# Performance work log

Measured on AMD Instinct MI355X. Metric: run time of the kernel, lower is better.

## Reference

```python
import jax, jax.numpy as jnp
import numpy as np

N_NODES = 100000
N_EDGES = 1600000
IN_FEATS = 128
N_HIDDEN = 128
N_CLASSES = 47


def _glorot(key, shape):
    lim = float(np.sqrt(6.0 / (shape[0] + shape[1])))
    return jax.random.uniform(key, shape, jnp.float32, -lim, lim)


def setup_inputs() -> dict:
    key = jax.random.key(0)
    ks = jax.random.split(key, 9)
    x = jax.random.normal(ks[0], (N_NODES, IN_FEATS), jnp.float32)
    src = jax.random.randint(ks[1], (N_EDGES,), 0, N_NODES, jnp.int32)
    dst = jax.random.randint(ks[2], (N_EDGES,), 0, N_NODES, jnp.int32)
    return {
        "x": x,
        "W_self_0": _glorot(ks[3], (IN_FEATS, N_HIDDEN)),
        "W_neigh_0": _glorot(ks[4], (IN_FEATS, N_HIDDEN)),
        "W_self_1": _glorot(ks[5], (N_HIDDEN, N_HIDDEN)),
        "W_neigh_1": _glorot(ks[6], (N_HIDDEN, N_HIDDEN)),
        "W_self_2": _glorot(ks[7], (N_HIDDEN, N_CLASSES)),
        "W_neigh_2": _glorot(ks[8], (N_HIDDEN, N_CLASSES)),
        "src": src,
        "dst": dst,
    }


def _sage_layer(h, src, dst, W_self, W_neigh):
    # mean aggregation of in-neighbor features (DGL SAGEConv 'mean', no bias)
    neigh_sum = jax.ops.segment_sum(h[src], dst, num_segments=N_NODES)  # [N, d]
    deg = jax.ops.segment_sum(jnp.ones((src.shape[0],), h.dtype), dst,
                              num_segments=N_NODES)  # [N]
    h_neigh = neigh_sum / jnp.maximum(deg, 1.0)[:, None]
    return h @ W_self + h_neigh @ W_neigh


def reference(x, W_self_0, W_neigh_0, W_self_1, W_neigh_1, W_self_2, W_neigh_2,
              src, dst):
    h = _sage_layer(x, src, dst, W_self_0, W_neigh_0)
    h = jax.nn.relu(h)  # dropout is identity in eval/reference mode
    h = _sage_layer(h, src, dst, W_self_1, W_neigh_1)
    h = jax.nn.relu(h)
    h = _sage_layer(h, src, dst, W_self_2, W_neigh_2)
    return h
```

## Files before the change

### kernel.cpp

```cpp
#include <hip/hip_runtime.h>
#include <hip/hip_bf16.h>

#define NN 100000
#define NE 1600000
#define NBK 196

typedef __attribute__((ext_vector_type(8))) short bf16x8;
typedef __attribute__((ext_vector_type(4))) float f32x4;

__device__ __forceinline__ unsigned short f2bf(float x) {
    unsigned u = __float_as_uint(x);
    return (unsigned short)((u + 0x7fffu + ((u >> 16) & 1u)) >> 16);
}
__device__ __forceinline__ float bflo(unsigned v) { return __uint_as_float(v << 16); }
__device__ __forceinline__ float bfhi(unsigned v) { return __uint_as_float(v & 0xffff0000u); }

#define ACCV(A, v) do { \
    A[0] += bflo((v).x); A[1] += bfhi((v).x); \
    A[2] += bflo((v).y); A[3] += bfhi((v).y); \
    A[4] += bflo((v).z); A[5] += bfhi((v).z); \
    A[6] += bflo((v).w); A[7] += bfhi((v).w); } while (0)

#define DRAIN(A, e, end) do { \
    for (; e + 15 < end; e += 16) { \
        int c0 = csr[e + g], c1 = csr[e + 4 + g], c2 = csr[e + 8 + g], c3 = csr[e + 12 + g]; \
        uint4 w0 = *(const uint4*)(hb + (unsigned)c0 + l16); \
        uint4 w1 = *(const uint4*)(hb + (unsigned)c1 + l16); \
        uint4 w2 = *(const uint4*)(hb + (unsigned)c2 + l16); \
        uint4 w3 = *(const uint4*)(hb + (unsigned)c3 + l16); \
        ACCV(A, w0); ACCV(A, w1); ACCV(A, w2); ACCV(A, w3); } \
    for (; e + 3 < end; e += 4) { \
        int c = csr[e + g]; \
        uint4 w = *(const uint4*)(hb + (unsigned)c + l16); \
        ACCV(A, w); } \
    { int rem = end - e; \
      if (g < rem) { \
        int c = csr[e + g]; \
        uint4 w = *(const uint4*)(hb + (unsigned)c + l16); \
        ACCV(A, w); } } \
} while (0)

__global__ void cast_x(const float* __restrict__ x, unsigned short* __restrict__ h, int n) {
    int i = (blockIdx.x * blockDim.x + threadIdx.x) * 4;
    if (i >= n) return;
    float4 v = *(const float4*)(x + i);
    unsigned out0 = ((unsigned)f2bf(v.y) << 16) | f2bf(v.x);
    unsigned out1 = ((unsigned)f2bf(v.w) << 16) | f2bf(v.z);
    *(uint2*)(h + i) = make_uint2(out0, out1);
}

__global__ __launch_bounds__(256) void hist_buck(const int* __restrict__ dst, int* __restrict__ bhist) {
    __shared__ int h[NBK];
    int t = threadIdx.x;
    if (t < NBK) h[t] = 0;
    __syncthreads();
    int base = blockIdx.x * 4096;
#pragma unroll
    for (int i = 0; i < 16; ++i) {
        int e = base + t + i * 256;
        if (e < NE) atomicAdd(&h[dst[e] >> 9], 1);
    }
    __syncthreads();
    if (t < NBK && h[t]) atomicAdd(&bhist[t], h[t]);
}

__global__ void scan_buck(const int* __restrict__ bhist, int* __restrict__ bbase,
                          int* __restrict__ gcur, int* __restrict__ row_ptr) {
    __shared__ int s[256];
    int t = threadIdx.x;
    int v = (t < NBK) ? bhist[t] : 0;
    s[t] = v;
    __syncthreads();
    for (int off = 1; off < 256; off <<= 1) {
        int u = (t >= off) ? s[t - off] : 0;
        __syncthreads();
        s[t] += u;
        __syncthreads();
    }
    int ex = s[t] - v;
    if (t <= NBK) bbase[t] = ex;
    if (t < NBK) gcur[t * 16] = ex;
    if (t == 0) row_ptr[NN] = NE;
}

__global__ __launch_bounds__(256) void sort_scatter(const int* __restrict__ src,
                                                    const int* __restrict__ dst,
                                                    int* __restrict__ gcur,
                                                    unsigned* __restrict__ pairs) {
    __shared__ int bcnt[NBK], gbase[NBK], lcur[NBK];
    int t = threadIdx.x;
    if (t < NBK) { bcnt[t] = 0; lcur[t] = 0; }
    __syncthreads();
    int base = blockIdx.x * 4096;
#pragma unroll
    for (int i = 0; i < 16; ++i) {
        int e = base + t + i * 256;
        if (e < NE) atomicAdd(&bcnt[dst[e] >> 9], 1);
    }
    __syncthreads();
    if (t < NBK) gbase[t] = atomicAdd(&gcur[t * 16], bcnt[t]);
    __syncthreads();
#pragma unroll
    for (int i = 0; i < 16; ++i) {
        int e = base + t + i * 256;
        if (e < NE) {
            int d = dst[e];
            int b = d >> 9;
            int p = atomicAdd(&lcur[b], 1);
            pairs[gbase[b] + p] = ((unsigned)src[e] << 9) | (unsigned)(d & 511);
        }
    }
}

__global__ __launch_bounds__(512) void bucket_place(const unsigned* __restrict__ pairs,
                                                    const int* __restrict__ bbase,
                                                    int* __restrict__ row_ptr,
                                                    float* __restrict__ inv_deg,
                                                    int* __restrict__ csr) {
    __shared__ int hist[512], sc[512], cur[512];
    int b = blockIdx.x, t = threadIdx.x;
    hist[t] = 0;
    __syncthreads();
    int beg = bbase[b], end = bbase[b + 1];
    for (int i = beg + t; i < end; i += 512) atomicAdd(&hist[pairs[i] & 511u], 1);
    __syncthreads();
    int deg = hist[t];
    sc[t] = deg;
    __syncthreads();
    for (int off = 1; off < 512; off <<= 1) {
        int u = (t >= off) ? sc[t - off] : 0;
        __syncthreads();
        sc[t] += u;
        __syncthreads();
    }
    int ex = sc[t] - deg;
    int node = b * 512 + t;
    if (node < NN) {
        row_ptr[node] = beg + ex;
        inv_deg[node] = 1.0f / (float)max(deg, 1);
    }
    cur[t] = beg + ex;
    __syncthreads();
    for (int i = beg + t; i < end; i += 512) {
        unsigned p = pairs[i];
        int pos = atomicAdd(&cur[p & 511u], 1);
        csr[pos] = (int)(p >> 9) << 8;
    }
}

__global__ void pack_w_all(const float* __restrict__ Ws0, const float* __restrict__ Wn0,
                           const float* __restrict__ Ws1, const float* __restrict__ Wn1,
                           const float* __restrict__ Ws2, const float* __restrict__ Wn2,
                           unsigned short* __restrict__ wp0, unsigned short* __restrict__ wp1,
                           unsigned short* __restrict__ wp2) {
    int idx = blockIdx.x * blockDim.x + threadIdx.x;
    const float *Ws, *Wn;
    unsigned short* wp;
    int Ncols, NF, local;
    if (idx < 32768)       { Ws = Ws0; Wn = Wn0; wp = wp0; Ncols = 128; NF = 8; local = idx; }
    else if (idx < 65536)  { Ws = Ws1; Wn = Wn1; wp = wp1; Ncols = 128; NF = 8; local = idx - 32768; }
    else if (idx < 77824)  { Ws = Ws2; Wn = Wn2; wp = wp2; Ncols = 47;  NF = 3; local = idx - 65536; }
    else return;
    int j = local & 7;
    int lane = (local >> 3) & 63;
    int fid = local >> 9;
    int nf = fid % NF;
    int kstep = fid / NF;
    int k = kstep * 32 + (lane >> 4) * 8 + j;
    int n = nf * 16 + (lane & 15);
    float v = 0.f;
    if (n < Ncols) v = (k < 128) ? Ws[k * Ncols + n] : Wn[(k - 128) * Ncols + n];
    wp[local] = f2bf(v);
}

__global__ __launch_bounds__(256) void aggregate(const unsigned* __restrict__ h32,
                                                 const int* __restrict__ csr,
                                                 const int* __restrict__ row_ptr,
                                                 const float* __restrict__ inv_deg,
                                                 unsigned* __restrict__ agg32) {
    int lane = threadIdx.x & 63;
    int wave = threadIdx.x >> 6;
    int n0 = (blockIdx.x * 4 + wave) * 2;
    if (n0 >= NN) return;
    int g = lane >> 4;
    unsigned l16 = (unsigned)(lane & 15) * 16;
    const char* hb = (const char*)h32;
    int b0  = row_ptr[n0];
    int m0  = row_ptr[n0 + 1];
    int e1e = row_ptr[n0 + 2];

    float a[8], b[8];
#pragma unroll
    for (int j = 0; j < 8; ++j) { a[j] = 0.f; b[j] = 0.f; }

    int e0 = b0, e1 = m0;
    while (e0 + 15 < m0 && e1 + 15 < e1e) {
        int c00 = csr[e0 + g], c01 = csr[e0 + 4 + g], c02 = csr[e0 + 8 + g], c03 = csr[e0 + 12 + g];
        int c10 = csr[e1 + g], c11 = csr[e1 + 4 + g], c12 = csr[e1 + 8 + g], c13 = csr[e1 + 12 + g];
        uint4 v00 = *(const uint4*)(hb + (unsigned)c00 + l16);
        uint4 v01 = *(const uint4*)(hb + (unsigned)c01 + l16);
        uint4 v02 = *(const uint4*)(hb + (unsigned)c02 + l16);
        uint4 v03 = *(const uint4*)(hb + (unsigned)c03 + l16);
        uint4 v10 = *(const uint4*)(hb + (unsigned)c10 + l16);
        uint4 v11 = *(const uint4*)(hb + (unsigned)c11 + l16);
        uint4 v12 = *(const uint4*)(hb + (unsigned)c12 + l16);
        uint4 v13 = *(const uint4*)(hb + (unsigned)c13 + l16);
        ACCV(a, v00); ACCV(a, v01); ACCV(a, v02); ACCV(a, v03);
        ACCV(b, v10); ACCV(b, v11); ACCV(b, v12); ACCV(b, v13);
        e0 += 16; e1 += 16;
    }
    DRAIN(a, e0, m0);
    DRAIN(b, e1, e1e);

#pragma unroll
    for (int j = 0; j < 8; ++j) {
        a[j] += __shfl_xor(a[j], 16, 64);
        a[j] += __shfl_xor(a[j], 32, 64);
        b[j] += __shfl_xor(b[j], 16, 64);
        b[j] += __shfl_xor(b[j], 32, 64);
    }
    float inv = inv_deg[n0 + ((lane >> 4) & 1)];
    if (lane < 32) {
        float r[8];
#pragma unroll
        for (int j = 0; j < 8; ++j) r[j] = ((lane < 16) ? a[j] : b[j]) * inv;
        unsigned d0 = ((unsigned)f2bf(r[1]) << 16) | f2bf(r[0]);
        unsigned d1 = ((unsigned)f2bf(r[3]) << 16) | f2bf(r[2]);
        unsigned d2 = ((unsigned)f2bf(r[5]) << 16) | f2bf(r[4]);
        unsigned d3 = ((unsigned)f2bf(r[7]) << 16) | f2bf(r[6]);
        int node = n0 + (lane >> 4);
        *(uint4*)((char*)agg32 + (size_t)node * 256 + l16) = make_uint4(d0, d1, d2, d3);
    }
}

template <int NF, bool LAST>
__global__ __launch_bounds__(256) void gemm_k(const unsigned short* __restrict__ hA,
                                              const unsigned short* __restrict__ hAgg,
                                              const unsigned short* __restrict__ wpack,
                                              unsigned short* __restrict__ hOut,
                                              float* __restrict__ fOut) {
    int lane = threadIdx.x & 63;
    int wave = threadIdx.x >> 6;
    int aRow = blockIdx.x * 64 + wave * 16 + (lane & 15);
    int kgrp = (lane >> 4) * 8;

    f32x4 acc[NF];
#pragma unroll
    for (int f = 0; f < NF; ++f)
#pragma unroll
        for (int q = 0; q < 4; ++q) acc[f][q] = 0.f;

    bool inb = (aRow < NN);
#pragma unroll
    for (int half = 0; half < 2; ++half) {
        const unsigned short* A = half ? hAgg : hA;
#pragma unroll
        for (int ks = 0; ks < 4; ++ks) {
            bf16x8 afrag;
            if (inb) {
                afrag = *(const bf16x8*)(A + (size_t)aRow * 128 + ks * 32 + kgrp);
            } else {
#pragma unroll
                for (int j = 0; j < 8; ++j) afrag[j] = 0;
            }
            int kstep = half * 4 + ks;
#pragma unroll
            for (int nf = 0; nf < NF; ++nf) {
                bf16x8 b = *(const bf16x8*)(wpack + (((kstep * NF + nf) * 64) + lane) * 8);
                acc[nf] = __builtin_amdgcn_mfma_f32_16x16x32_bf16(afrag, b, acc[nf], 0, 0, 0);
            }
        }
    }

    int col0 = lane & 15;
    int rBase = blockIdx.x * 64 + wave * 16 + (lane >> 4) * 4;
#pragma unroll
    for (int nf = 0; nf < NF; ++nf) {
        int col = nf * 16 + col0;
        if (LAST) {
            if (col < 47) {
#pragma unroll
                for (int q = 0; q < 4; ++q) {
                    int row = rBase + q;
                    if (row < NN) fOut[(size_t)row * 47 + col] = acc[nf][q];
                }
            }
        } else {
#pragma unroll
            for (int q = 0; q < 4; ++q) {
                int row = rBase + q;
                if (row < NN) hOut[(size_t)row * 128 + col] = f2bf(fmaxf(acc[nf][q], 0.f));
            }
        }
    }
}

static inline size_t alignup(size_t x) { return (x + 255) & ~(size_t)255; }

extern "C" void kernel_launch(void* const* d_in, const int* in_sizes, int n_in,
                              void* d_out, int out_size, void* d_ws, size_t ws_size,
                              hipStream_t stream) {
    const float* x   = (const float*)d_in[0];
    const float* Ws0 = (const float*)d_in[1];
    const float* Wn0 = (const float*)d_in[2];
    const float* Ws1 = (const float*)d_in[3];
    const float* Wn1 = (const float*)d_in[4];
    const float* Ws2 = (const float*)d_in[5];
    const float* Wn2 = (const float*)d_in[6];
    const int* src   = (const int*)d_in[7];
    const int* dst   = (const int*)d_in[8];
    float* out = (float*)d_out;

    char* w = (char*)d_ws;
    size_t off = 0;
    int* row_ptr   = (int*)(w + off);   off += alignup((NN + 1) * 4);
    int* bhist     = (int*)(w + off);   off += alignup(NBK * 4);
    int* bbase     = (int*)(w + off);   off += alignup((NBK + 1) * 4);
    int* gcur      = (int*)(w + off);   off += alignup((size_t)NBK * 16 * 4);
    float* inv_deg = (float*)(w + off); off += alignup(NN * 4);
    int* csr       = (int*)(w + off);   off += alignup((size_t)NE * 4);
    unsigned* pairs = (unsigned*)(w + off); off += alignup((size_t)NE * 4);
    unsigned short* wp0 = (unsigned short*)(w + off); off += alignup(8 * 8 * 64 * 8 * 2);
    unsigned short* wp1 = (unsigned short*)(w + off); off += alignup(8 * 8 * 64 * 8 * 2);
    unsigned short* wp2 = (unsigned short*)(w + off); off += alignup(8 * 3 * 64 * 8 * 2);
    unsigned short* hA  = (unsigned short*)(w + off); off += alignup((size_t)NN * 128 * 2);
    unsigned short* hB  = (unsigned short*)(w + off); off += alignup((size_t)NN * 128 * 2);
    unsigned short* agg = (unsigned short*)(w + off); off += alignup((size_t)NN * 128 * 2);

    hipMemsetAsync(bhist, 0, NBK * 4, stream);

    cast_x<<<dim3((NN * 128 / 4 + 255) / 256), dim3(256), 0, stream>>>(x, hA, NN * 128);
    hist_buck<<<dim3((NE + 4095) / 4096), dim3(256), 0, stream>>>(dst, bhist);
    scan_buck<<<dim3(1), dim3(256), 0, stream>>>(bhist, bbase, gcur, row_ptr);
    sort_scatter<<<dim3((NE + 4095) / 4096), dim3(256), 0, stream>>>(src, dst, gcur, pairs);
    bucket_place<<<dim3(NBK), dim3(512), 0, stream>>>(pairs, bbase, row_ptr, inv_deg, csr);

    pack_w_all<<<dim3((77824 + 255) / 256), dim3(256), 0, stream>>>(
        Ws0, Wn0, Ws1, Wn1, Ws2, Wn2, wp0, wp1, wp2);

    const int aggGrid  = (NN / 2 + 3) / 4;
    const int gemmGrid = (NN + 63) / 64;

    aggregate<<<dim3(aggGrid), dim3(256), 0, stream>>>((const unsigned*)hA, csr, row_ptr, inv_deg, (unsigned*)agg);
    gemm_k<8, false><<<dim3(gemmGrid), dim3(256), 0, stream>>>(hA, agg, wp0, hB, nullptr);
    aggregate<<<dim3(aggGrid), dim3(256), 0, stream>>>((const unsigned*)hB, csr, row_ptr, inv_deg, (unsigned*)agg);
    gemm_k<8, false><<<dim3(gemmGrid), dim3(256), 0, stream>>>(hB, agg, wp1, hA, nullptr);
    aggregate<<<dim3(aggGrid), dim3(256), 0, stream>>>((const unsigned*)hA, csr, row_ptr, inv_deg, (unsigned*)agg);
    gemm_k<3, true><<<dim3(gemmGrid), dim3(256), 0, stream>>>(hA, agg, wp2, nullptr, out);
}
```

Measured before the change: 388.6 us.

## Remap aggregate and GEMM blocks for XCD locality, merge scan with weight pack

Aggregation moves from two nodes per wave to one node per wave, and block indices are remapped so each of the 8 XCDs works on a contiguous node range. The GEMM block order gets the same XCD-aware swizzle. The bucket sort switches to 256-node buckets (391 buckets, 256-thread place kernel), and the bucket scan is fused with weight packing into one launch. The goals are better L2 locality per XCD, fewer kernel launches and smaller per-bucket work. The cost is less memory-level parallelism per wave in aggregation.

```diff
diff --git a/kernel.cpp b/kernel.cpp
--- a/kernel.cpp
+++ b/kernel.cpp
@@ -3,7 +3,7 @@
 
 #define NN 100000
 #define NE 1600000
-#define NBK 196
+#define NBK 391
 
 typedef __attribute__((ext_vector_type(8))) short bf16x8;
 typedef __attribute__((ext_vector_type(4))) float f32x4;
@@ -21,24 +21,11 @@
     A[4] += bflo((v).z); A[5] += bfhi((v).z); \
     A[6] += bflo((v).w); A[7] += bfhi((v).w); } while (0)
 
-#define DRAIN(A, e, end) do { \
-    for (; e + 15 < end; e += 16) { \
-        int c0 = csr[e + g], c1 = csr[e + 4 + g], c2 = csr[e + 8 + g], c3 = csr[e + 12 + g]; \
-        uint4 w0 = *(const uint4*)(hb + (unsigned)c0 + l16); \
-        uint4 w1 = *(const uint4*)(hb + (unsigned)c1 + l16); \
-        uint4 w2 = *(const uint4*)(hb + (unsigned)c2 + l16); \
-        uint4 w3 = *(const uint4*)(hb + (unsigned)c3 + l16); \
-        ACCV(A, w0); ACCV(A, w1); ACCV(A, w2); ACCV(A, w3); } \
-    for (; e + 3 < end; e += 4) { \
-        int c = csr[e + g]; \
-        uint4 w = *(const uint4*)(hb + (unsigned)c + l16); \
-        ACCV(A, w); } \
-    { int rem = end - e; \
-      if (g < rem) { \
-        int c = csr[e + g]; \
-        uint4 w = *(const uint4*)(hb + (unsigned)c + l16); \
-        ACCV(A, w); } } \
-} while (0)
+__device__ __forceinline__ int swz8(int i, int nwg) {
+    int q = nwg >> 3, r = nwg & 7;
+    int x = i & 7, j = i >> 3;
+    return (x < r) ? x * (q + 1) + j : r * (q + 1) + (x - r) * q + j;
+}
 
 __global__ void cast_x(const float* __restrict__ x, unsigned short* __restrict__ h, int n) {
     int i = (blockIdx.x * blockDim.x + threadIdx.x) * 4;
@@ -52,115 +39,51 @@
 __global__ __launch_bounds__(256) void hist_buck(const int* __restrict__ dst, int* __restrict__ bhist) {
     __shared__ int h[NBK];
     int t = threadIdx.x;
-    if (t < NBK) h[t] = 0;
+    for (int i = t; i < NBK; i += 256) h[i] = 0;
     __syncthreads();
     int base = blockIdx.x * 4096;
 #pragma unroll
     for (int i = 0; i < 16; ++i) {
         int e = base + t + i * 256;
-        if (e < NE) atomicAdd(&h[dst[e] >> 9], 1);
-    }
-    __syncthreads();
-    if (t < NBK && h[t]) atomicAdd(&bhist[t], h[t]);
-}
-
-__global__ void scan_buck(const int* __restrict__ bhist, int* __restrict__ bbase,
-                          int* __restrict__ gcur, int* __restrict__ row_ptr) {
-    __shared__ int s[256];
+        if (e < NE) atomicAdd(&h[dst[e] >> 8], 1);
+    }
+    __syncthreads();
+    for (int i = t; i < NBK; i += 256)
+        if (h[i]) atomicAdd(&bhist[i], h[i]);
+}
+
+__global__ __launch_bounds__(512) void scan_pack(const int* __restrict__ bhist, int* __restrict__ bbase,
+                                                 int* __restrict__ gcur, int* __restrict__ row_ptr,
+                                                 const float* __restrict__ Ws0, const float* __restrict__ Wn0,
+                                                 const float* __restrict__ Ws1, const float* __restrict__ Wn1,
+                                                 const float* __restrict__ Ws2, const float* __restrict__ Wn2,
+                                                 unsigned short* __restrict__ wp0, unsigned short* __restrict__ wp1,
+                                                 unsigned short* __restrict__ wp2) {
     int t = threadIdx.x;
-    int v = (t < NBK) ? bhist[t] : 0;
-    s[t] = v;
-    __syncthreads();
-    for (int off = 1; off < 256; off <<= 1) {
-        int u = (t >= off) ? s[t - off] : 0;
+    if (blockIdx.x == 0) {
+        __shared__ int s[512];
+        int v = (t < NBK) ? bhist[t] : 0;
+        s[t] = v;
         __syncthreads();
-        s[t] += u;
-        __syncthreads();
-    }
-    int ex = s[t] - v;
-    if (t <= NBK) bbase[t] = ex;
-    if (t < NBK) gcur[t * 16] = ex;
-    if (t == 0) row_ptr[NN] = NE;
-}
-
-__global__ __launch_bounds__(256) void sort_scatter(const int* __restrict__ src,
-                                                    const int* __restrict__ dst,
-                                                    int* __restrict__ gcur,
-                                                    unsigned* __restrict__ pairs) {
-    __shared__ int bcnt[NBK], gbase[NBK], lcur[NBK];
-    int t = threadIdx.x;
-    if (t < NBK) { bcnt[t] = 0; lcur[t] = 0; }
-    __syncthreads();
-    int base = blockIdx.x * 4096;
-#pragma unroll
-    for (int i = 0; i < 16; ++i) {
-        int e = base + t + i * 256;
-        if (e < NE) atomicAdd(&bcnt[dst[e] >> 9], 1);
-    }
-    __syncthreads();
-    if (t < NBK) gbase[t] = atomicAdd(&gcur[t * 16], bcnt[t]);
-    __syncthreads();
-#pragma unroll
-    for (int i = 0; i < 16; ++i) {
-        int e = base + t + i * 256;
-        if (e < NE) {
-            int d = dst[e];
-            int b = d >> 9;
-            int p = atomicAdd(&lcur[b], 1);
-            pairs[gbase[b] + p] = ((unsigned)src[e] << 9) | (unsigned)(d & 511);
+        for (int off = 1; off < 512; off <<= 1) {
+            int u = (t >= off) ? s[t - off] : 0;
+            __syncthreads();
+            s[t] += u;
+            __syncthreads();
         }
-    }
-}
-
-__global__ __launch_bounds__(512) void bucket_place(const unsigned* __restrict__ pairs,
-                                                    const int* __restrict__ bbase,
-                                                    int* __restrict__ row_ptr,
-                                                    float* __restrict__ inv_deg,
-                                                    int* __restrict__ csr) {
-    __shared__ int hist[512], sc[512], cur[512];
-    int b = blockIdx.x, t = threadIdx.x;
-    hist[t] = 0;
-    __syncthreads();
-    int beg = bbase[b], end = bbase[b + 1];
-    for (int i = beg + t; i < end; i += 512) atomicAdd(&hist[pairs[i] & 511u], 1);
-    __syncthreads();
-    int deg = hist[t];
-    sc[t] = deg;
-    __syncthreads();
-    for (int off = 1; off < 512; off <<= 1) {
-        int u = (t >= off) ? sc[t - off] : 0;
-        __syncthreads();
-        sc[t] += u;
-        __syncthreads();
-    }
-    int ex = sc[t] - deg;
-    int node = b * 512 + t;
-    if (node < NN) {
-        row_ptr[node] = beg + ex;
-        inv_deg[node] = 1.0f / (float)max(deg, 1);
-    }
-    cur[t] = beg + ex;
-    __syncthreads();
-    for (int i = beg + t; i < end; i += 512) {
-        unsigned p = pairs[i];
-        int pos = atomicAdd(&cur[p & 511u], 1);
-        csr[pos] = (int)(p >> 9) << 8;
-    }
-}
-
-__global__ void pack_w_all(const float* __restrict__ Ws0, const float* __restrict__ Wn0,
-                           const float* __restrict__ Ws1, const float* __restrict__ Wn1,
-                           const float* __restrict__ Ws2, const float* __restrict__ Wn2,
-                           unsigned short* __restrict__ wp0, unsigned short* __restrict__ wp1,
-                           unsigned short* __restrict__ wp2) {
-    int idx = blockIdx.x * blockDim.x + threadIdx.x;
+        int ex = s[t] - v;
+        if (t <= NBK) bbase[t] = ex;
+        if (t < NBK) gcur[t * 16] = ex;
+        if (t == 0) row_ptr[NN] = NE;
+        return;
+    }
+    int local = (blockIdx.x - 1) * 512 + t;
     const float *Ws, *Wn;
     unsigned short* wp;
-    int Ncols, NF, local;
-    if (idx < 32768)       { Ws = Ws0; Wn = Wn0; wp = wp0; Ncols = 128; NF = 8; local = idx; }
-    else if (idx < 65536)  { Ws = Ws1; Wn = Wn1; wp = wp1; Ncols = 128; NF = 8; local = idx - 32768; }
-    else if (idx < 77824)  { Ws = Ws2; Wn = Wn2; wp = wp2; Ncols = 47;  NF = 3; local = idx - 65536; }
-    else return;
+    int Ncols, NF;
+    if (local < 32768)      { Ws = Ws0; Wn = Wn0; wp = wp0; Ncols = 128; NF = 8; }
+    else if (local < 65536) { Ws = Ws1; Wn = Wn1; wp = wp1; Ncols = 128; NF = 8; local -= 32768; }
+    else                    { Ws = Ws2; Wn = Wn2; wp = wp2; Ncols = 47;  NF = 3; local -= 65536; }
     int j = local & 7;
     int lane = (local >> 3) & 63;
     int fid = local >> 9;
@@ -173,6 +96,72 @@
     wp[local] = f2bf(v);
 }
 
+__global__ __launch_bounds__(256) void sort_scatter(const int* __restrict__ src,
+                                                    const int* __restrict__ dst,
+                                                    int* __restrict__ gcur,
+                                                    unsigned* __restrict__ pairs) {
+    __shared__ int bcnt[NBK], gbase[NBK], lcur[NBK];
+    int t = threadIdx.x;
+    for (int i = t; i < NBK; i += 256) { bcnt[i] = 0; lcur[i] = 0; }
+    __syncthreads();
+    int base = blockIdx.x * 4096;
+#pragma unroll
+    for (int i = 0; i < 16; ++i) {
+        int e = base + t + i * 256;
+        if (e < NE) atomicAdd(&bcnt[dst[e] >> 8], 1);
+    }
+    __syncthreads();
+    for (int i = t; i < NBK; i += 256)
+        if (bcnt[i]) gbase[i] = atomicAdd(&gcur[i * 16], bcnt[i]);
+    __syncthreads();
+#pragma unroll
+    for (int i = 0; i < 16; ++i) {
+        int e = base + t + i * 256;
+        if (e < NE) {
+            int d = dst[e];
+            int b = d >> 8;
+            int p = atomicAdd(&lcur[b], 1);
+            pairs[gbase[b] + p] = ((unsigned)src[e] << 8) | (unsigned)(d & 255);
+        }
+    }
+}
+
+__global__ __launch_bounds__(256) void bucket_place(const unsigned* __restrict__ pairs,
+                                                    const int* __restrict__ bbase,
+                                                    int* __restrict__ row_ptr,
+                                                    float* __restrict__ inv_deg,
+                                                    int* __restrict__ csr) {
+    __shared__ int hist[256], sc[256], cur[256];
+    int b = blockIdx.x, t = threadIdx.x;
+    hist[t] = 0;
+    __syncthreads();
+    int beg = bbase[b], end = bbase[b + 1];
+    for (int i = beg + t; i < end; i += 256) atomicAdd(&hist[pairs[i] & 255u], 1);
+    __syncthreads();
+    int deg = hist[t];
+    sc[t] = deg;
+    __syncthreads();
+    for (int off = 1; off < 256; off <<= 1) {
+        int u = (t >= off) ? sc[t - off] : 0;
+        __syncthreads();
+        sc[t] += u;
+        __syncthreads();
+    }
+    int ex = sc[t] - deg;
+    int node = b * 256 + t;
+    if (node < NN) {
+        row_ptr[node] = beg + ex;
+        inv_deg[node] = 1.0f / (float)max(deg, 1);
+    }
+    cur[t] = beg + ex;
+    __syncthreads();
+    for (int i = beg + t; i < end; i += 256) {
+        unsigned p = pairs[i];
+        int pos = atomicAdd(&cur[p & 255u], 1);
+        csr[pos] = (int)(p & 0xFFFFFF00u);
+    }
+}
+
 __global__ __launch_bounds__(256) void aggregate(const unsigned* __restrict__ h32,
                                                  const int* __restrict__ csr,
                                                  const int* __restrict__ row_ptr,
@@ -180,55 +169,51 @@
                                                  unsigned* __restrict__ agg32) {
     int lane = threadIdx.x & 63;
     int wave = threadIdx.x >> 6;
-    int n0 = (blockIdx.x * 4 + wave) * 2;
-    if (n0 >= NN) return;
+    int chunk = (blockIdx.x & 7) * 3125 + (blockIdx.x >> 3);
+    int node = chunk * 4 + wave;
     int g = lane >> 4;
     unsigned l16 = (unsigned)(lane & 15) * 16;
     const char* hb = (const char*)h32;
-    int b0  = row_ptr[n0];
-    int m0  = row_ptr[n0 + 1];
-    int e1e = row_ptr[n0 + 2];
-
-    float a[8], b[8];
-#pragma unroll
-    for (int j = 0; j < 8; ++j) { a[j] = 0.f; b[j] = 0.f; }
-
-    int e0 = b0, e1 = m0;
-    while (e0 + 15 < m0 && e1 + 15 < e1e) {
-        int c00 = csr[e0 + g], c01 = csr[e0 + 4 + g], c02 = csr[e0 + 8 + g], c03 = csr[e0 + 12 + g];
-        int c10 = csr[e1 + g], c11 = csr[e1 + 4 + g], c12 = csr[e1 + 8 + g], c13 = csr[e1 + 12 + g];
-        uint4 v00 = *(const uint4*)(hb + (unsigned)c00 + l16);
-        uint4 v01 = *(const uint4*)(hb + (unsigned)c01 + l16);
-        uint4 v02 = *(const uint4*)(hb + (unsigned)c02 + l16);
-        uint4 v03 = *(const uint4*)(hb + (unsigned)c03 + l16);
-        uint4 v10 = *(const uint4*)(hb + (unsigned)c10 + l16);
-        uint4 v11 = *(const uint4*)(hb + (unsigned)c11 + l16);
-        uint4 v12 = *(const uint4*)(hb + (unsigned)c12 + l16);
-        uint4 v13 = *(const uint4*)(hb + (unsigned)c13 + l16);
-        ACCV(a, v00); ACCV(a, v01); ACCV(a, v02); ACCV(a, v03);
-        ACCV(b, v10); ACCV(b, v11); ACCV(b, v12); ACCV(b, v13);
-        e0 += 16; e1 += 16;
-    }
-    DRAIN(a, e0, m0);
-    DRAIN(b, e1, e1e);
+    int beg = row_ptr[node], end = row_ptr[node + 1];
+    float acc[8];
+#pragma unroll
+    for (int j = 0; j < 8; ++j) acc[j] = 0.f;
+
+    int e = beg;
+    for (; e + 15 < end; e += 16) {
+        int c0 = csr[e + g];
+        int c1 = csr[e + 4 + g];
+        int c2 = csr[e + 8 + g];
+        int c3 = csr[e + 12 + g];
+        uint4 v0 = *(const uint4*)(hb + (unsigned)c0 + l16);
+        uint4 v1 = *(const uint4*)(hb + (unsigned)c1 + l16);
+        uint4 v2 = *(const uint4*)(hb + (unsigned)c2 + l16);
+        uint4 v3 = *(const uint4*)(hb + (unsigned)c3 + l16);
+        ACCV(acc, v0); ACCV(acc, v1); ACCV(acc, v2); ACCV(acc, v3);
+    }
+    for (; e + 3 < end; e += 4) {
+        int c = csr[e + g];
+        uint4 v = *(const uint4*)(hb + (unsigned)c + l16);
+        ACCV(acc, v);
+    }
+    int rem = end - e;
+    if (g < rem) {
+        int c = csr[e + g];
+        uint4 v = *(const uint4*)(hb + (unsigned)c + l16);
+        ACCV(acc, v);
+    }
 
 #pragma unroll
     for (int j = 0; j < 8; ++j) {
-        a[j] += __shfl_xor(a[j], 16, 64);
-        a[j] += __shfl_xor(a[j], 32, 64);
-        b[j] += __shfl_xor(b[j], 16, 64);
-        b[j] += __shfl_xor(b[j], 32, 64);
-    }
-    float inv = inv_deg[n0 + ((lane >> 4) & 1)];
-    if (lane < 32) {
-        float r[8];
-#pragma unroll
-        for (int j = 0; j < 8; ++j) r[j] = ((lane < 16) ? a[j] : b[j]) * inv;
-        unsigned d0 = ((unsigned)f2bf(r[1]) << 16) | f2bf(r[0]);
-        unsigned d1 = ((unsigned)f2bf(r[3]) << 16) | f2bf(r[2]);
-        unsigned d2 = ((unsigned)f2bf(r[5]) << 16) | f2bf(r[4]);
-        unsigned d3 = ((unsigned)f2bf(r[7]) << 16) | f2bf(r[6]);
-        int node = n0 + (lane >> 4);
+        acc[j] += __shfl_xor(acc[j], 16, 64);
+        acc[j] += __shfl_xor(acc[j], 32, 64);
+    }
+    float inv = inv_deg[node];
+    if (lane < 16) {
+        unsigned d0 = ((unsigned)f2bf(acc[1] * inv) << 16) | f2bf(acc[0] * inv);
+        unsigned d1 = ((unsigned)f2bf(acc[3] * inv) << 16) | f2bf(acc[2] * inv);
+        unsigned d2 = ((unsigned)f2bf(acc[5] * inv) << 16) | f2bf(acc[4] * inv);
+        unsigned d3 = ((unsigned)f2bf(acc[7] * inv) << 16) | f2bf(acc[6] * inv);
         *(uint4*)((char*)agg32 + (size_t)node * 256 + l16) = make_uint4(d0, d1, d2, d3);
     }
 }
@@ -241,7 +226,9 @@
                                               float* __restrict__ fOut) {
     int lane = threadIdx.x & 63;
     int wave = threadIdx.x >> 6;
-    int aRow = blockIdx.x * 64 + wave * 16 + (lane & 15);
+    int chunk = swz8(blockIdx.x, (int)gridDim.x);
+    int base = chunk * 64;
+    int aRow = base + wave * 16 + (lane & 15);
     int kgrp = (lane >> 4) * 8;
 
     f32x4 acc[NF];
@@ -273,7 +260,7 @@
     }
 
     int col0 = lane & 15;
-    int rBase = blockIdx.x * 64 + wave * 16 + (lane >> 4) * 4;
+    int rBase = base + wave * 16 + (lane >> 4) * 4;
 #pragma unroll
     for (int nf = 0; nf < NF; ++nf) {
         int col = nf * 16 + col0;
@@ -331,14 +318,12 @@
 
     cast_x<<<dim3((NN * 128 / 4 + 255) / 256), dim3(256), 0, stream>>>(x, hA, NN * 128);
     hist_buck<<<dim3((NE + 4095) / 4096), dim3(256), 0, stream>>>(dst, bhist);
-    scan_buck<<<dim3(1), dim3(256), 0, stream>>>(bhist, bbase, gcur, row_ptr);
+    scan_pack<<<dim3(153), dim3(512), 0, stream>>>(bhist, bbase, gcur, row_ptr,
+                                                   Ws0, Wn0, Ws1, Wn1, Ws2, Wn2, wp0, wp1, wp2);
     sort_scatter<<<dim3((NE + 4095) / 4096), dim3(256), 0, stream>>>(src, dst, gcur, pairs);
-    bucket_place<<<dim3(NBK), dim3(512), 0, stream>>>(pairs, bbase, row_ptr, inv_deg, csr);
-
-    pack_w_all<<<dim3((77824 + 255) / 256), dim3(256), 0, stream>>>(
-        Ws0, Wn0, Ws1, Wn1, Ws2, Wn2, wp0, wp1, wp2);
-
-    const int aggGrid  = (NN / 2 + 3) / 4;
+    bucket_place<<<dim3(NBK), dim3(256), 0, stream>>>(pairs, bbase, row_ptr, inv_deg, csr);
+
+    const int aggGrid  = NN / 4;
     const int gemmGrid = (NN + 63) / 64;
 
     aggregate<<<dim3(aggGrid), dim3(256), 0, stream>>>((const unsigned*)hA, csr, row_ptr, inv_deg, (unsigned*)agg);
```

Result: faster. 334.3 us (-14.0%).
